# Kernel tuning notes

Hardware: AMD Instinct MI355X
Metric: run time of the kernel (lower is better)

The kernel has to match this reference:

```python
import jax, jax.numpy as jnp
import numpy as np

B, H, W, C = 8, 32, 32, 512
NUM_HEADS = 8
HEAD_DIM = C // NUM_HEADS
SCALE = HEAD_DIM ** -0.5


def setup_inputs() -> dict:
    key = jax.random.key(0)
    ks = jax.random.split(key, 10)
    s = 0.02
    return {
        "x": jax.random.normal(ks[0], (B, H, W, C), dtype=jnp.float32),
        "qkv_w": jax.random.normal(ks[1], (3 * C, C), dtype=jnp.float32) * s,
        "proj_w": jax.random.normal(ks[2], (C, C), dtype=jnp.float32) * s,
        "proj_b": jnp.zeros((C,), dtype=jnp.float32),
        "fconv_w": jax.random.normal(ks[3], (C,), dtype=jnp.float32) * s,
        "fconv_b": jnp.zeros((C,), dtype=jnp.float32),
        "freq_w": jnp.ones((C,), dtype=jnp.float32),
        "ln_g": jnp.ones((C,), dtype=jnp.float32),
        "ln_b": jnp.zeros((C,), dtype=jnp.float32),
        "mix_w": jnp.array([0.5, 0.5], dtype=jnp.float32),
    }


def _spatial(x, qkv_w, proj_w, proj_b):
    b, h, w, c = x.shape
    n = h * w
    xf = x.reshape(b, n, c)
    qkv = xf @ qkv_w.T                                   # [b,n,3c]
    qkv = qkv.reshape(b, n, 3, NUM_HEADS, HEAD_DIM)
    q, k, v = qkv[:, :, 0], qkv[:, :, 1], qkv[:, :, 2]   # [b,n,h,d]
    attn = jnp.einsum("bqhd,bkhd->bhqk", q, k) * SCALE
    attn = jax.nn.softmax(attn, axis=-1)
    out = jnp.einsum("bhqk,bkhd->bqhd", attn, v).reshape(b, n, c)
    out = out @ proj_w.T + proj_b
    return out.reshape(b, h, w, c)


def _fourier(x, fconv_w, fconv_b, freq_w, ln_g, ln_b):
    b, h, w, c = x.shape
    xc = jnp.transpose(x, (0, 3, 1, 2))                  # [b,c,h,w]
    xfft = jnp.fft.rfft2(xc, norm="ortho")               # [b,c,h,w//2+1] complex
    enhanced = xfft * freq_w[None, :, None, None]
    # depthwise 1x1 conv applied to real and imag separately: y = x*w + bias
    wc = fconv_w[None, :, None, None]
    bc = fconv_b[None, :, None, None]
    fconv = xfft * wc + bc * (1.0 + 1.0j)
    combined = enhanced + 0.1 * fconv
    xif = jnp.fft.irfft2(combined, s=(h, w), norm="ortho")  # [b,c,h,w]
    xf = jnp.transpose(xif, (0, 2, 3, 1))                # [b,h,w,c]
    mu = jnp.mean(xf, axis=-1, keepdims=True)
    var = jnp.var(xf, axis=-1, keepdims=True)
    return (xf - mu) / jnp.sqrt(var + 1e-5) * ln_g + ln_b


def reference(x, qkv_w, proj_w, proj_b, fconv_w, fconv_b, freq_w, ln_g, ln_b, mix_w):
    spatial = _spatial(x, qkv_w, proj_w, proj_b)
    fourier = _fourier(x, fconv_w, fconv_b, freq_w, ln_g, ln_b)
    weights = jax.nn.softmax(mix_w)
    return weights[0] * spatial + weights[1] * fourier
```

## Files before the change

### kernel.cpp

```cpp
#include <hip/hip_runtime.h>

typedef unsigned short u16;
typedef __attribute__((ext_vector_type(8))) short bfrag;
typedef __attribute__((ext_vector_type(4))) float f32x4;
typedef __attribute__((ext_vector_type(4))) int i32x4;
typedef __attribute__((ext_vector_type(4))) unsigned short us4;
typedef __attribute__((ext_vector_type(8))) unsigned short us8;

__device__ __forceinline__ u16 f2bf(float f){
  unsigned int u = __float_as_uint(f);
  u += 0x7fffu + ((u >> 16) & 1u);
  return (u16)(u >> 16);
}

__global__ __launch_bounds__(256) void cast_all(const float* __restrict__ x,
    const float* __restrict__ wq, const float* __restrict__ wp,
    u16* __restrict__ xb, u16* __restrict__ wqb, u16* __restrict__ wpb)
{
  long e = ((long)blockIdx.x * 256 + threadIdx.x) * 4;
  const float* src; u16* dst; long off;
  if (e < 4194304L)               { src = x;  dst = xb;  off = e; }
  else if (e < 4980736L)          { src = wq; dst = wqb; off = e - 4194304L; }
  else                            { src = wp; dst = wpb; off = e - 4980736L; }
  f32x4 v = *(const f32x4*)(src + off);
  us4 o; o[0]=f2bf(v[0]); o[1]=f2bf(v[1]); o[2]=f2bf(v[2]); o[3]=f2bf(v[3]);
  *(us4*)(dst + off) = o;
}

__device__ __forceinline__ void gemm_core_128(const u16* __restrict__ A,
    const u16* __restrict__ W, int K, int m0, int n0,
    u16* As, u16* Ws, f32x4 acc[4][4])
{
  const int t = threadIdx.x;
  const int lane = t & 63, wave = t >> 6;
  const int wr = wave >> 1, wc = wave & 1;
  const int l15 = lane & 15, l4 = lane >> 4;
  for (int k0 = 0; k0 < K; k0 += 32){
    __syncthreads();
    #pragma unroll
    for (int i = 0; i < 2; i++){
      int idx = t + i*256;
      int row = idx >> 2, c8 = (idx & 3) * 8;
      *(i32x4*)&As[idx*8] = *(const i32x4*)&A[(long)(m0+row)*K + k0 + c8];
      *(i32x4*)&Ws[idx*8] = *(const i32x4*)&W[(long)(n0+row)*K + k0 + c8];
    }
    __syncthreads();
    bfrag af[4], wf[4];
    #pragma unroll
    for (int m = 0; m < 4; m++) af[m] = *(bfrag*)&As[(wr*64 + m*16 + l15)*32 + l4*8];
    #pragma unroll
    for (int n = 0; n < 4; n++) wf[n] = *(bfrag*)&Ws[(wc*64 + n*16 + l15)*32 + l4*8];
    #pragma unroll
    for (int m = 0; m < 4; m++)
      #pragma unroll
      for (int n = 0; n < 4; n++)
        acc[m][n] = __builtin_amdgcn_mfma_f32_16x16x32_bf16(af[m], wf[n], acc[m][n], 0, 0, 0);
  }
}

__global__ __launch_bounds__(256) void gemm_qkv(const u16* __restrict__ A,
    const u16* __restrict__ W, u16* __restrict__ Qb, u16* __restrict__ Kb, u16* __restrict__ Vt)
{
  __shared__ __align__(16) u16 As[128*32];
  __shared__ __align__(16) u16 Ws[128*32];
  f32x4 acc[4][4] = {};
  const int m0 = blockIdx.y * 128, n0 = blockIdx.x * 128;
  gemm_core_128(A, W, 512, m0, n0, As, Ws, acc);
  const int lane = threadIdx.x & 63, wave = threadIdx.x >> 6;
  const int wr = wave >> 1, wc = wave & 1, l15 = lane & 15, l4 = lane >> 4;
  #pragma unroll
  for (int m = 0; m < 4; m++)
    #pragma unroll
    for (int n = 0; n < 4; n++){
      int col = n0 + wc*64 + n*16 + l15;
      int s = col >> 9, r9 = col & 511;
      int hh = r9 >> 6, dd = r9 & 63;
      int row0 = m0 + wr*64 + m*16 + l4*4;
      int bb = row0 >> 10, nn = row0 & 1023;
      if (s == 2){
        us4 o;
        #pragma unroll
        for (int r = 0; r < 4; r++) o[r] = f2bf(acc[m][n][r]);
        *(us4*)&Vt[((long)(bb*8 + hh)*64 + dd)*1024 + nn] = o;
      } else {
        u16* base = (s == 0) ? Qb : Kb;
        #pragma unroll
        for (int r = 0; r < 4; r++)
          base[((long)(bb*8 + hh)*1024 + nn + r)*64 + dd] = f2bf(acc[m][n][r]);
      }
    }
}

__global__ __launch_bounds__(256) void gemm_proj(const u16* __restrict__ A,
    const u16* __restrict__ W, const float* __restrict__ bias, float* __restrict__ C)
{
  __shared__ __align__(16) u16 As[128*32];
  __shared__ __align__(16) u16 Ws[128*32];
  f32x4 acc[4][4] = {};
  const int m0 = blockIdx.y * 128, n0 = blockIdx.x * 128;
  gemm_core_128(A, W, 512, m0, n0, As, Ws, acc);
  const int lane = threadIdx.x & 63, wave = threadIdx.x >> 6;
  const int wr = wave >> 1, wc = wave & 1, l15 = lane & 15, l4 = lane >> 4;
  #pragma unroll
  for (int m = 0; m < 4; m++)
    #pragma unroll
    for (int n = 0; n < 4; n++){
      int col = n0 + wc*64 + n*16 + l15;
      float bv = bias[col];
      #pragma unroll
      for (int r = 0; r < 4; r++){
        int row = m0 + wr*64 + m*16 + l4*4 + r;
        C[(long)row*512 + col] = acc[m][n][r] + bv;
      }
    }
}

__global__ __launch_bounds__(256) void attn_kernel(const u16* __restrict__ Qb,
    const u16* __restrict__ Kb, const u16* __restrict__ Vt, u16* __restrict__ attn_out)
{
  const int qt = blockIdx.x;
  const int bh = blockIdx.y;
  const int b = bh >> 3, h = bh & 7;
  const int t = threadIdx.x;
  const int wave = t >> 6, lane = t & 63;
  const int l15 = lane & 15, l4 = lane >> 4;
  __shared__ __align__(16) u16 Ks[64][72];
  __shared__ __align__(16) u16 Vs[64][72];
  __shared__ __align__(16) u16 Ps[4][16][72];

  bfrag aq[2];
  const u16* Qbase = Qb + ((long)bh*1024 + qt*64 + wave*16) * 64;
  #pragma unroll
  for (int kd = 0; kd < 2; kd++)
    aq[kd] = *(const bfrag*)(Qbase + l15*64 + kd*32 + l4*8);

  f32x4 accO[4] = {};
  float lsum[4] = {0.f, 0.f, 0.f, 0.f};
  const float cexp = 0.125f * 1.4426950408889634f;

  const u16* Kbh = Kb + (long)bh*1024*64;
  const u16* Vbh = Vt + (long)bh*64*1024;

  for (int kt = 0; kt < 16; kt++){
    __syncthreads();
    #pragma unroll
    for (int i = 0; i < 2; i++){
      int idx = t + i*256; int r = idx >> 3, c8 = (idx & 7) * 8;
      i32x4 kv = *(const i32x4*)(Kbh + (long)(kt*64 + r)*64 + c8);
      i32x4 vv = *(const i32x4*)(Vbh + (long)r*1024 + kt*64 + c8);
      *(i32x4*)&Ks[r][c8] = kv;
      *(i32x4*)&Vs[r][c8] = vv;
    }
    __syncthreads();
    #pragma unroll
    for (int kf = 0; kf < 4; kf++){
      f32x4 a = {};
      #pragma unroll
      for (int kd = 0; kd < 2; kd++){
        bfrag bk = *(bfrag*)&Ks[kf*16 + l15][kd*32 + l4*8];
        a = __builtin_amdgcn_mfma_f32_16x16x32_bf16(aq[kd], bk, a, 0, 0, 0);
      }
      #pragma unroll
      for (int r = 0; r < 4; r++){
        float p = exp2f(a[r] * cexp);
        lsum[r] += p;
        Ps[wave][l4*4 + r][kf*16 + l15] = f2bf(p);
      }
    }
    __syncthreads();
    #pragma unroll
    for (int h2 = 0; h2 < 2; h2++){
      bfrag pa = *(bfrag*)&Ps[wave][l15][h2*32 + l4*8];
      #pragma unroll
      for (int df = 0; df < 4; df++){
        bfrag bv = *(bfrag*)&Vs[df*16 + l15][h2*32 + l4*8];
        accO[df] = __builtin_amdgcn_mfma_f32_16x16x32_bf16(pa, bv, accO[df], 0, 0, 0);
      }
    }
  }
  #pragma unroll
  for (int r = 0; r < 4; r++){
    #pragma unroll
    for (int off = 1; off < 16; off <<= 1) lsum[r] += __shfl_xor(lsum[r], off, 64);
    float inv = 1.0f / lsum[r];
    int nq = qt*64 + wave*16 + l4*4 + r;
    u16* dst = attn_out + ((long)(b*1024 + nq))*512 + h*64;
    #pragma unroll
    for (int df = 0; df < 4; df++)
      dst[df*16 + l15] = f2bf(accO[df][r] * inv);
  }
}

__global__ __launch_bounds__(256) void fourier_mix(const float* __restrict__ x,
    const float* __restrict__ spatial,
    const float* __restrict__ fconv_w, const float* __restrict__ fconv_b,
    const float* __restrict__ freq_w, const float* __restrict__ ln_g,
    const float* __restrict__ ln_b, const float* __restrict__ mix_w,
    float* __restrict__ out)
{
  const int row = blockIdx.x * 4 + (threadIdx.x >> 6);
  const int lane = threadIdx.x & 63;
  const int c0 = lane * 8;
  const float* xr = x + (long)row*512 + c0;
  f32x4 xlo = *(const f32x4*)xr;
  f32x4 xhi = *(const f32x4*)(xr + 4);
  float xv[8] = {xlo[0],xlo[1],xlo[2],xlo[3],xhi[0],xhi[1],xhi[2],xhi[3]};
  const int hh = (row >> 5) & 31, ww = row & 31;
  float pw = 0.0f;
  if (hh == 0){
    pw = 1.0f + ((ww & 1) ? -1.0f : 1.0f);
    for (int k = 1; k < 16; k++){
      float ang = 6.283185307179586f * (float)(k*ww) / 32.0f;
      pw += 2.0f * (__cosf(ang) - __sinf(ang));
    }
  }
  float sum = 0.0f, ssq = 0.0f;
  float xf[8];
  #pragma unroll
  for (int j = 0; j < 8; j++){
    int c = c0 + j;
    float s = freq_w[c] + 0.1f * fconv_w[c];
    float v = xv[j]*s + 0.1f * fconv_b[c] * pw;
    xf[j] = v; sum += v; ssq += v*v;
  }
  #pragma unroll
  for (int off = 1; off < 64; off <<= 1){
    sum += __shfl_xor(sum, off, 64);
    ssq += __shfl_xor(ssq, off, 64);
  }
  const float mean = sum * (1.0f/512.0f);
  const float var  = ssq * (1.0f/512.0f) - mean*mean;
  const float rstd = rsqrtf(var + 1e-5f);
  const float e0 = expf(mix_w[0]), e1 = expf(mix_w[1]);
  const float w0 = e0/(e0+e1), w1 = e1/(e0+e1);
  const float* sp = spatial + (long)row*512 + c0;
  f32x4 olo, ohi;
  #pragma unroll
  for (int j = 0; j < 8; j++){
    int c = c0 + j;
    float ln = (xf[j] - mean)*rstd*ln_g[c] + ln_b[c];
    float o = w0*sp[j] + w1*ln;
    if (j < 4) olo[j] = o; else ohi[j-4] = o;
  }
  float* od = out + (long)row*512 + c0;
  *(f32x4*)od = olo;
  *(f32x4*)(od + 4) = ohi;
}

extern "C" void kernel_launch(void* const* d_in, const int* in_sizes, int n_in,
                              void* d_out, int out_size, void* d_ws, size_t ws_size,
                              hipStream_t stream)
{
  const float* x       = (const float*)d_in[0];
  const float* qkv_w   = (const float*)d_in[1];
  const float* proj_w  = (const float*)d_in[2];
  const float* proj_b  = (const float*)d_in[3];
  const float* fconv_w = (const float*)d_in[4];
  const float* fconv_b = (const float*)d_in[5];
  const float* freq_w  = (const float*)d_in[6];
  const float* ln_g    = (const float*)d_in[7];
  const float* ln_b    = (const float*)d_in[8];
  const float* mix_w   = (const float*)d_in[9];

  char* ws = (char*)d_ws;
  u16*   xb      = (u16*)(ws + 0);
  u16*   wqb     = (u16*)(ws + 8388608);
  u16*   wpb     = (u16*)(ws + 9961472);
  u16*   Qb      = (u16*)(ws + 10485760);
  u16*   Kb      = (u16*)(ws + 18874368);
  u16*   Vt      = (u16*)(ws + 27262976);
  u16*   attn    = (u16*)(ws + 35651584);
  float* spatial = (float*)(ws + 44040192);
  float* outp    = (float*)d_out;

  cast_all<<<dim3(5120), dim3(256), 0, stream>>>(x, qkv_w, proj_w, xb, wqb, wpb);
  gemm_qkv<<<dim3(12, 64), dim3(256), 0, stream>>>(xb, wqb, Qb, Kb, Vt);
  attn_kernel<<<dim3(16, 64), dim3(256), 0, stream>>>(Qb, Kb, Vt, attn);
  gemm_proj<<<dim3(4, 64), dim3(256), 0, stream>>>(attn, wpb, proj_b, spatial);
  fourier_mix<<<dim3(2048), dim3(256), 0, stream>>>(x, spatial, fconv_w, fconv_b,
                                                    freq_w, ln_g, ln_b, mix_w, outp);
}
```

Measured before the change: 177.8 us.

## Prefetch K/V tiles in registers and use direct global-to-LDS loads in GEMM

In the GEMM core, the tiles are now copied straight from global memory into LDS with global_load_lds, so they no longer pass through registers. In the attention kernel, the next K/V tile is loaded into registers while the current tile is being computed. The full __syncthreads calls are replaced by raw s_barrier plus an explicit lgkmcnt wait, and the barrier between writing P and reading it is dropped because each wave only touches its own P buffer. The goal is to hide global memory latency and cut synchronisation overhead. The cost is more register pressure and reliance on hand-written waitcnt and barrier semantics being correct.

```diff
diff --git a/kernel.cpp b/kernel.cpp
--- a/kernel.cpp
+++ b/kernel.cpp
@@ -41,8 +41,12 @@
     for (int i = 0; i < 2; i++){
       int idx = t + i*256;
       int row = idx >> 2, c8 = (idx & 3) * 8;
-      *(i32x4*)&As[idx*8] = *(const i32x4*)&A[(long)(m0+row)*K + k0 + c8];
-      *(i32x4*)&Ws[idx*8] = *(const i32x4*)&W[(long)(n0+row)*K + k0 + c8];
+      __builtin_amdgcn_global_load_lds(
+        (const __attribute__((address_space(1))) void*)(A + (long)(m0+row)*K + k0 + c8),
+        (__attribute__((address_space(3))) void*)(As + idx*8), 16, 0, 0);
+      __builtin_amdgcn_global_load_lds(
+        (const __attribute__((address_space(1))) void*)(W + (long)(n0+row)*K + k0 + c8),
+        (__attribute__((address_space(3))) void*)(Ws + idx*8), 16, 0, 0);
     }
     __syncthreads();
     bfrag af[4], wf[4];
@@ -141,17 +145,33 @@
   const u16* Kbh = Kb + (long)bh*1024*64;
   const u16* Vbh = Vt + (long)bh*64*1024;
 
+  const int sr = t >> 3;
+  const int sc = (t & 7) * 8;
+  i32x4 kreg[2], vreg[2];
+  #pragma unroll
+  for (int i = 0; i < 2; i++){
+    int r = sr + i*32;
+    kreg[i] = *(const i32x4*)(Kbh + (long)r*64 + sc);
+    vreg[i] = *(const i32x4*)(Vbh + (long)r*1024 + sc);
+  }
+
   for (int kt = 0; kt < 16; kt++){
-    __syncthreads();
+    asm volatile("s_barrier" ::: "memory");
     #pragma unroll
     for (int i = 0; i < 2; i++){
-      int idx = t + i*256; int r = idx >> 3, c8 = (idx & 7) * 8;
-      i32x4 kv = *(const i32x4*)(Kbh + (long)(kt*64 + r)*64 + c8);
-      i32x4 vv = *(const i32x4*)(Vbh + (long)r*1024 + kt*64 + c8);
-      *(i32x4*)&Ks[r][c8] = kv;
-      *(i32x4*)&Vs[r][c8] = vv;
-    }
-    __syncthreads();
+      int r = sr + i*32;
+      *(i32x4*)&Ks[r][sc] = kreg[i];
+      *(i32x4*)&Vs[r][sc] = vreg[i];
+    }
+    if (kt < 15){
+      #pragma unroll
+      for (int i = 0; i < 2; i++){
+        int r = sr + i*32;
+        kreg[i] = *(const i32x4*)(Kbh + (long)((kt+1)*64 + r)*64 + sc);
+        vreg[i] = *(const i32x4*)(Vbh + (long)r*1024 + (kt+1)*64 + sc);
+      }
+    }
+    asm volatile("s_waitcnt lgkmcnt(0)\ns_barrier" ::: "memory");
     #pragma unroll
     for (int kf = 0; kf < 4; kf++){
       f32x4 a = {};
@@ -167,7 +187,6 @@
         Ps[wave][l4*4 + r][kf*16 + l15] = f2bf(p);
       }
     }
-    __syncthreads();
     #pragma unroll
     for (int h2 = 0; h2 < 2; h2++){
       bfrag pa = *(bfrag*)&Ps[wave][l15][h2*32 + l4*8];
```

Result: no change. 174.8 us (-1.7%).
